# Kernel tuning notes

Hardware: AMD Instinct MI355X
Metric: run time of the kernel (lower is better)

## Reference

```python
import math
import jax, jax.numpy as jnp
import numpy as np

B, T, C, H = 2, 2048, 1024, 16
D = C // H


def _slopes(n):
    def p2(m):
        start = 2 ** (-(2 ** -(math.log2(m) - 3)))
        return [start * start ** i for i in range(m)]
    if math.log2(n).is_integer():
        return p2(n)
    c = 2 ** math.floor(math.log2(n))
    return p2(c) + _slopes(2 * c)[0::2][: n - c]


def setup_inputs() -> dict:
    key = jax.random.key(0)
    ks = jax.random.split(key, 9)
    std = 0.02
    x = jax.random.normal(ks[0], (B, T, C), dtype=jnp.float32)
    Wq = std * jax.random.normal(ks[1], (C, C), dtype=jnp.float32)
    Wk = std * jax.random.normal(ks[2], (C, C), dtype=jnp.float32)
    Wv = std * jax.random.normal(ks[3], (C, C), dtype=jnp.float32)
    # fc_resid init: std 0.02/sqrt(num_layers)
    Wo = (std / math.sqrt(24.0)) * jax.random.normal(ks[4], (C, C), dtype=jnp.float32)
    bq = jnp.zeros((C,), jnp.float32)
    bk = jnp.zeros((C,), jnp.float32)
    bv = jnp.zeros((C,), jnp.float32)
    bo = jnp.zeros((C,), jnp.float32)
    return {"x": x, "Wq": Wq, "bq": bq, "Wk": Wk, "bk": bk,
            "Wv": Wv, "bv": bv, "Wo": Wo, "bo": bo}


def reference(x, Wq, bq, Wk, bk, Wv, bv, Wo, bo):
    # projections -> [B, T, H, D]
    q = (x @ Wq + bq).reshape(B, T, H, D)
    k = (x @ Wk + bk).reshape(B, T, H, D)
    v = (x @ Wv + bv).reshape(B, T, H, D)

    scale = 1.0 / math.sqrt(D)
    att = jnp.einsum("bqhd,bkhd->bhqk", q, k) * scale  # [B,H,T,T]

    slopes = jnp.asarray(_slopes(H), dtype=jnp.float32)  # [H]
    i = jnp.arange(T)
    rel = i[None, :] - i[None, :].T  # rel[i,j] = j - i
    causal = rel <= 0  # j <= i
    # alibi bias: -tril(i - j) = tril(j - i), scaled per head
    alibi = slopes[:, None, None] * jnp.where(causal, rel, 0).astype(jnp.float32)

    att = att + alibi[None]  # broadcast over batch
    att = jnp.where(causal[None, None], att, -jnp.inf)
    att = jax.nn.softmax(att, axis=-1)

    y = jnp.einsum("bhqk,bkhd->bqhd", att, v).reshape(B, T, C)
    return y @ Wo + bo  # dropout p=0 (eval) is identity
```

## Files before the change

kernel.cpp:

```cpp
#include <hip/hip_runtime.h>
#include <hip/hip_bf16.h>

typedef __bf16 bf16;
typedef __bf16 bf16x4 __attribute__((ext_vector_type(4)));
typedef __bf16 bf16x8 __attribute__((ext_vector_type(8)));
typedef float floatx4 __attribute__((ext_vector_type(4)));
typedef short short4_ __attribute__((ext_vector_type(4)));

#define B_ 2
#define T_ 2048
#define C_ 1024
#define H_ 16
#define D_ 64
#define M_ 4096
#define QK_LD 2048

__device__ __forceinline__ void load_lds16(const void* g, void* l) {
  __builtin_amdgcn_global_load_lds(
      (const __attribute__((address_space(1))) unsigned int*)g,
      (__attribute__((address_space(3))) unsigned int*)l, 16, 0, 0);
}

__device__ __forceinline__ floatx4 mfma16(bf16x4 a, bf16x4 b, floatx4 c) {
#if __has_builtin(__builtin_amdgcn_mfma_f32_16x16x16_bf16)
  return __builtin_amdgcn_mfma_f32_16x16x16_bf16(a, b, c, 0, 0, 0);
#else
  return __builtin_amdgcn_mfma_f32_16x16x16bf16_1k(
      __builtin_bit_cast(short4_, a), __builtin_bit_cast(short4_, b), c, 0, 0, 0);
#endif
}

struct PrepArgs { const float* w[4]; bf16* wt[4]; const float* x; bf16* xb; };

__global__ __launch_bounds__(256)
void prep(PrepArgs p) {
  const int bid = blockIdx.x;
  if (bid < 4096) {
    __shared__ float tile[32][33];
    const int z = bid >> 10, xy = bid & 1023;
    const int bx = xy & 31, by = xy >> 5;
    const float* in = p.w[z];
    bf16* out = p.wt[z];
    int tx = threadIdx.x & 31, ty = threadIdx.x >> 5;
    int n0 = bx * 32, k0 = by * 32;
#pragma unroll
    for (int j = 0; j < 32; j += 8)
      tile[ty + j][tx] = in[(size_t)(k0 + ty + j) * C_ + n0 + tx];
    __syncthreads();
#pragma unroll
    for (int j = 0; j < 32; j += 8)
      out[(size_t)(n0 + ty + j) * C_ + k0 + tx] = (bf16)tile[tx][ty + j];
  } else {
    int i = ((bid - 4096) * 256 + threadIdx.x) * 8;
    float4 a = *(const float4*)(p.x + i);
    float4 b = *(const float4*)(p.x + i + 4);
    bf16x8 o;
    o[0] = (bf16)a.x; o[1] = (bf16)a.y; o[2] = (bf16)a.z; o[3] = (bf16)a.w;
    o[4] = (bf16)b.x; o[5] = (bf16)b.y; o[6] = (bf16)b.z; o[7] = (bf16)b.w;
    *(bf16x8*)(p.xb + i) = o;
  }
}

struct GQ {
  const bf16* A; const bf16* Bt;
  const float* bias[3];
  bf16* Cout; bf16* vt; int N; int K;
};

__global__ __launch_bounds__(256, 2)
void gemm128(GQ g) {
  __shared__ __align__(16) bf16 As[128 * 64];
  __shared__ __align__(16) bf16 Bs[128 * 64];
  const int tid = threadIdx.x;
  const int wave = tid >> 6, lane = tid & 63;
  const int quad = lane >> 4, l16 = lane & 15;
  const int m0 = blockIdx.y * 128, n0 = blockIdx.x * 128;
  const int wm = (wave >> 1) * 64, wn = (wave & 1) * 64;

  floatx4 acc[4][4] = {};

  int rA[4], cA[4];
#pragma unroll
  for (int t = 0; t < 4; ++t) {
    int pch = (wave * 4 + t) * 64 + lane;
    rA[t] = pch >> 3;
    cA[t] = (pch & 7) ^ (rA[t] & 7);
  }

  for (int k0 = 0; k0 < g.K; k0 += 64) {
    __syncthreads();
#pragma unroll
    for (int t = 0; t < 4; ++t) {
      load_lds16(g.A + (size_t)(m0 + rA[t]) * g.K + k0 + cA[t] * 8,
                 As + (wave * 4 + t) * 512);
      load_lds16(g.Bt + (size_t)(n0 + rA[t]) * g.K + k0 + cA[t] * 8,
                 Bs + (wave * 4 + t) * 512);
    }
    __builtin_amdgcn_s_waitcnt(0x0f70);
    __syncthreads();
#pragma unroll
    for (int s = 0; s < 2; ++s) {
      bf16x8 af[4], bfr[4];
#pragma unroll
      for (int i = 0; i < 4; ++i) {
        int mr = wm + i * 16 + l16;
        af[i] = *(const bf16x8*)(As + ((mr * 8) + ((s * 4 + quad) ^ (mr & 7))) * 8);
        int nr = wn + i * 16 + l16;
        bfr[i] = *(const bf16x8*)(Bs + ((nr * 8) + ((s * 4 + quad) ^ (nr & 7))) * 8);
      }
#pragma unroll
      for (int i = 0; i < 4; ++i)
#pragma unroll
        for (int j = 0; j < 4; ++j)
          acc[i][j] = __builtin_amdgcn_mfma_f32_16x16x32_bf16(af[i], bfr[j],
                                                              acc[i][j], 0, 0, 0);
    }
  }

  const bool vsplit = (n0 >= 2048);
#pragma unroll
  for (int j = 0; j < 4; ++j) {
    int col = n0 + wn + j * 16 + l16;
    const float* bp = g.bias[col >> 10];
    float bv = bp[col & 1023];
    if (vsplit) {
      int cv = col - 2048;
      bf16* dst0 = g.vt + ((size_t)((m0 >> 11) * 16 + (cv >> 6)) * 64 + (cv & 63)) * (size_t)T_
                   + (m0 & 2047) + wm + quad * 4;
#pragma unroll
      for (int i = 0; i < 4; ++i) {
        bf16x4 pk;
#pragma unroll
        for (int r = 0; r < 4; ++r) pk[r] = (bf16)(acc[i][j][r] + bv);
        *(bf16x4*)(dst0 + i * 16) = pk;
      }
    } else {
#pragma unroll
      for (int i = 0; i < 4; ++i) {
#pragma unroll
        for (int r = 0; r < 4; ++r) {
          int row = m0 + wm + i * 16 + quad * 4 + r;
          g.Cout[(size_t)row * g.N + col] = (bf16)(acc[i][j][r] + bv);
        }
      }
    }
  }
}

__global__ __launch_bounds__(256, 2)
void gemm_out(const bf16* __restrict__ A, const bf16* __restrict__ Bt,
              const float* __restrict__ bias, float* __restrict__ C) {
  __shared__ __align__(16) bf16 As[64 * 64];
  __shared__ __align__(16) bf16 Bs[128 * 64];
  const int tid = threadIdx.x;
  const int wave = tid >> 6, lane = tid & 63;
  const int quad = lane >> 4, l16 = lane & 15;
  const int m0 = blockIdx.y * 64, n0 = blockIdx.x * 128;
  const int wm = (wave >> 1) * 32, wn = (wave & 1) * 64;

  floatx4 acc[2][4] = {};

  int rA[2], cA[2], rB[4], cB[4];
#pragma unroll
  for (int t = 0; t < 2; ++t) {
    int p = t * 256 + tid;
    rA[t] = p >> 3; cA[t] = (p & 7) ^ (rA[t] & 7);
  }
#pragma unroll
  for (int t = 0; t < 4; ++t) {
    int p = t * 256 + tid;
    rB[t] = p >> 3; cB[t] = (p & 7) ^ (rB[t] & 7);
  }

  for (int k0 = 0; k0 < 1024; k0 += 64) {
    __syncthreads();
#pragma unroll
    for (int t = 0; t < 2; ++t)
      load_lds16(A + (size_t)(m0 + rA[t]) * 1024 + k0 + cA[t] * 8,
                 As + t * 2048 + wave * 512);
#pragma unroll
    for (int t = 0; t < 4; ++t)
      load_lds16(Bt + (size_t)(n0 + rB[t]) * 1024 + k0 + cB[t] * 8,
                 Bs + t * 2048 + wave * 512);
    __builtin_amdgcn_s_waitcnt(0x0f70);
    __syncthreads();
#pragma unroll
    for (int s = 0; s < 2; ++s) {
      bf16x8 af[2], bfr[4];
#pragma unroll
      for (int i = 0; i < 2; ++i) {
        int mr = wm + i * 16 + l16;
        af[i] = *(const bf16x8*)(As + ((mr * 8) + ((s * 4 + quad) ^ (mr & 7))) * 8);
      }
#pragma unroll
      for (int j = 0; j < 4; ++j) {
        int nr = wn + j * 16 + l16;
        bfr[j] = *(const bf16x8*)(Bs + ((nr * 8) + ((s * 4 + quad) ^ (nr & 7))) * 8);
      }
#pragma unroll
      for (int i = 0; i < 2; ++i)
#pragma unroll
        for (int j = 0; j < 4; ++j)
          acc[i][j] = __builtin_amdgcn_mfma_f32_16x16x32_bf16(af[i], bfr[j],
                                                              acc[i][j], 0, 0, 0);
    }
  }

#pragma unroll
  for (int j = 0; j < 4; ++j) {
    int col = n0 + wn + j * 16 + l16;
    float bv = bias[col];
#pragma unroll
    for (int i = 0; i < 2; ++i)
#pragma unroll
      for (int r = 0; r < 4; ++r) {
        int row = m0 + wm + i * 16 + quad * 4 + r;
        C[(size_t)row * 1024 + col] = acc[i][j][r] + bv;
      }
  }
}

__constant__ int yy_map[24] = {7, 8, 16, 9, 17, 6, 10, 18, 11, 19, 5, 12,
                               20, 13, 21, 4, 14, 22, 15, 23, 3, 2, 1, 0};

__global__ __launch_bounds__(512, 2)
void attn8(const bf16* __restrict__ qk, const bf16* __restrict__ vt,
           bf16* __restrict__ y, bf16* __restrict__ po, float* __restrict__ pl) {
  __shared__ __align__(16) bf16 smem[17408];
  const int tid = threadIdx.x, wave = tid >> 6, lane = tid & 63;
  const int quad = lane >> 4, l16 = lane & 15;
  const int qs = wave >> 1, kh = wave & 1;
  const int bh = blockIdx.x, b = bh >> 4, h = bh & 15;
  const int yy = yy_map[blockIdx.y];
  int qb, kbeg, kcnt, seg;
  if (yy < 8)       { qb = yy;      kbeg = 0;      kcnt = 2 * qb + 2; seg = -1; }
  else if (yy < 16) { qb = 23 - yy; kbeg = 0;      kcnt = qb + 1;     seg = 0;  }
  else              { qb = 31 - yy; kbeg = qb + 1; kcnt = qb + 1;     seg = 1;  }

  const float L2E = 1.4426950408889634f;
  const float slope2 = exp2f(-0.5f * (float)(h + 1)) * L2E;
  const float scl2 = 0.125f * L2E;
  const float M0 = 14.0f;

  const int rS = tid >> 3;
  const int cS = (tid & 7) ^ (rS & 7);
  const bf16* kbase = qk + (size_t)b * T_ * QK_LD + 1024 + h * 64;
  const bf16* vbase = vt + (size_t)bh * 64 * T_;

  const int q0 = qb * 128;
  const int w0 = q0 + qs * 32;

  bf16x8 qf[2][2];
#pragma unroll
  for (int qt = 0; qt < 2; ++qt)
#pragma unroll
    for (int s = 0; s < 2; ++s)
      qf[qt][s] = *(const bf16x8*)(qk +
          (size_t)(b * T_ + w0 + qt * 16 + l16) * QK_LD + h * 64 + s * 32 + quad * 8);

  const int qi0 = w0 + l16;
  float qoff[2];
  qoff[0] = slope2 * (float)qi0 + M0;
  qoff[1] = qoff[0] + slope2 * 16.0f;
  float kc[2][4];
#pragma unroll
  for (int kt = 0; kt < 2; ++kt)
#pragma unroll
    for (int r = 0; r < 4; ++r)
      kc[kt][r] = slope2 * (float)(kt * 16 + quad * 4 + r);

  floatx4 o[2][4];
#pragma unroll
  for (int qt = 0; qt < 2; ++qt)
#pragma unroll
    for (int n = 0; n < 4; ++n) o[qt][n] = (floatx4)0.f;
  float lsum[2] = {0.f, 0.f};

  load_lds16(kbase + (size_t)(kbeg * 64 + rS) * QK_LD + cS * 8, smem + wave * 512);
  load_lds16(vbase + (size_t)rS * T_ + kbeg * 64 + cS * 8, smem + 8192 + wave * 512);
  __builtin_amdgcn_s_waitcnt(0x0f70);
  __syncthreads();

  for (int it = 0; it < kcnt; ++it) {
    const int kj0 = (kbeg + it) * 64;
    const int cur = it & 1;

    if (it + 1 < kcnt) {
      const int nk = kj0 + 64;
      load_lds16(kbase + (size_t)(nk + rS) * QK_LD + cS * 8,
                 smem + (cur ^ 1) * 4096 + wave * 512);
      load_lds16(vbase + (size_t)rS * T_ + nk + cS * 8,
                 smem + 8192 + (cur ^ 1) * 4096 + wave * 512);
    }

    const bf16* Klc = smem + cur * 4096;
    const bf16* Vlc = smem + 8192 + cur * 4096;

    bf16x8 kf[2][2];
#pragma unroll
    for (int ss = 0; ss < 2; ++ss)
#pragma unroll
      for (int kt = 0; kt < 2; ++kt) {
        const int krow = kh * 32 + kt * 16 + l16;
        kf[ss][kt] = *(const bf16x8*)(Klc + krow * 64 +
                                      (((ss * 4 + quad) ^ (krow & 7)) * 8));
      }
    bf16x4 vfr[4][2];
#pragma unroll
    for (int nt = 0; nt < 4; ++nt) {
      const int drow = nt * 16 + l16;
#pragma unroll
      for (int kt = 0; kt < 2; ++kt) {
        const int chunk = (kh * 4 + kt * 2 + (quad >> 1)) ^ (drow & 7);
        vfr[nt][kt] = *(const bf16x4*)(Vlc + drow * 64 + chunk * 8 + (quad & 1) * 4);
      }
    }

    const int kbi = kj0 + kh * 32;
    const float kb = slope2 * (float)kbi;

#pragma unroll
    for (int qt = 0; qt < 2; ++qt) {
      const int rb = w0 + qt * 16;
      floatx4 st[2] = {};
#pragma unroll
      for (int ss = 0; ss < 2; ++ss)
#pragma unroll
        for (int kt = 0; kt < 2; ++kt)
          st[kt] = __builtin_amdgcn_mfma_f32_16x16x32_bf16(kf[ss][kt], qf[qt][ss],
                                                           st[kt], 0, 0, 0);

      const float bb = kb - qoff[qt];
      const int qi = qi0 + qt * 16;
      bf16x4 pb[2];
      if (kbi + 31 > rb) {
#pragma unroll
        for (int kt = 0; kt < 2; ++kt) {
#pragma unroll
          for (int r = 0; r < 4; ++r) {
            float p = __builtin_amdgcn_exp2f(
                fmaf(st[kt][r], scl2, bb + kc[kt][r]));
            if (kbi + kt * 16 + quad * 4 + r > qi) p = 0.f;
            lsum[qt] += p;
            pb[kt][r] = (bf16)p;
          }
        }
      } else {
#pragma unroll
        for (int kt = 0; kt < 2; ++kt) {
#pragma unroll
          for (int r = 0; r < 4; ++r) {
            float p = __builtin_amdgcn_exp2f(
                fmaf(st[kt][r], scl2, bb + kc[kt][r]));
            lsum[qt] += p;
            pb[kt][r] = (bf16)p;
          }
        }
      }

#pragma unroll
      for (int nt = 0; nt < 4; ++nt)
#pragma unroll
        for (int kt = 0; kt < 2; ++kt)
          o[qt][nt] = mfma16(vfr[nt][kt], pb[kt], o[qt][nt]);
    }

    __builtin_amdgcn_s_waitcnt(0x0f70);
    __syncthreads();
  }

  float* Cb = (float*)smem;
  if (kh == 1) {
#pragma unroll
    for (int qt = 0; qt < 2; ++qt) {
#pragma unroll
      for (int n = 0; n < 4; ++n)
        *(floatx4*)(Cb + (((qs * 2 + qt) * 4 + n) * 64 + lane) * 4) = o[qt][n];
      Cb[8192 + (qs * 2 + qt) * 64 + lane] = lsum[qt];
    }
  }
  __syncthreads();
  if (kh == 1) return;
#pragma unroll
  for (int qt = 0; qt < 2; ++qt) {
#pragma unroll
    for (int n = 0; n < 4; ++n)
      o[qt][n] += *(const floatx4*)(Cb + (((qs * 2 + qt) * 4 + n) * 64 + lane) * 4);
    lsum[qt] += Cb[8192 + (qs * 2 + qt) * 64 + lane];
    lsum[qt] += __shfl_xor(lsum[qt], 16);
    lsum[qt] += __shfl_xor(lsum[qt], 32);
  }

  if (seg < 0) {
#pragma unroll
    for (int qt = 0; qt < 2; ++qt) {
      const float inv = 1.f / lsum[qt];
      bf16* yp = y + (size_t)(b * T_ + w0 + qt * 16 + l16) * C_ + h * 64 + quad * 4;
#pragma unroll
      for (int nt = 0; nt < 4; ++nt) {
        bf16x4 pk;
#pragma unroll
        for (int r = 0; r < 4; ++r) pk[r] = (bf16)(o[qt][nt][r] * inv);
        *(bf16x4*)(yp + nt * 16) = pk;
      }
    }
  } else {
    const int pid = (bh * 8 + (qb - 8)) * 2 + seg;
    bf16* pob = po + (size_t)pid * 8192;
#pragma unroll
    for (int qt = 0; qt < 2; ++qt) {
#pragma unroll
      for (int half = 0; half < 2; ++half) {
        bf16x8 pk;
#pragma unroll
        for (int jj = 0; jj < 8; ++jj)
          pk[jj] = (bf16)o[qt][half * 2 + (jj >> 2)][jj & 3];
        *(bf16x8*)(pob + (qt * 2 + half) * 2048 + (qs * 64 + lane) * 8) = pk;
      }
      if (quad == 0)
        pl[pid * 128 + qs * 32 + qt * 16 + l16] = lsum[qt];
    }
  }
}

__global__ __launch_bounds__(256)
void combine(const bf16* __restrict__ po, const float* __restrict__ pl,
             bf16* __restrict__ y) {
  const int x = blockIdx.x;
  const int bh = x >> 3, qb = (x & 7) + 8;
  const int b = bh >> 4, h = bh & 15;
  const int pid0 = (bh * 8 + (qb - 8)) * 2;
  const bf16* p0 = po + (size_t)pid0 * 8192;
  const bf16* p1 = p0 + 8192;
  const int t = threadIdx.x;
  const int qs = t >> 6, quad = (t >> 4) & 3, l16 = t & 15;

  float linv[2];
  int row[2];
#pragma unroll
  for (int qt = 0; qt < 2; ++qt) {
    row[qt] = qs * 32 + qt * 16 + l16;
    linv[qt] = 1.f / (pl[pid0 * 128 + row[qt]] + pl[(pid0 + 1) * 128 + row[qt]]);
  }

#pragma unroll
  for (int qt = 0; qt < 2; ++qt)
#pragma unroll
    for (int half = 0; half < 2; ++half) {
      bf16x8 a = *(const bf16x8*)(p0 + (qt * 2 + half) * 2048 + t * 8);
      bf16x8 c = *(const bf16x8*)(p1 + (qt * 2 + half) * 2048 + t * 8);
#pragma unroll
      for (int g = 0; g < 2; ++g) {
        bf16x4 outv;
#pragma unroll
        for (int r = 0; r < 4; ++r)
          outv[r] = (bf16)(((float)a[g * 4 + r] + (float)c[g * 4 + r]) * linv[qt]);
        const int col = (half * 2 + g) * 16 + quad * 4;
        *(bf16x4*)(y + (size_t)(b * T_ + qb * 128 + row[qt]) * C_ + h * 64 + col) = outv;
      }
    }
}

extern "C" void kernel_launch(void* const* d_in, const int* in_sizes, int n_in,
                              void* d_out, int out_size, void* d_ws, size_t ws_size,
                              hipStream_t stream) {
  const float* x  = (const float*)d_in[0];
  const float* Wq = (const float*)d_in[1];
  const float* bq = (const float*)d_in[2];
  const float* Wk = (const float*)d_in[3];
  const float* bk = (const float*)d_in[4];
  const float* Wv = (const float*)d_in[5];
  const float* bv = (const float*)d_in[6];
  const float* Wo = (const float*)d_in[7];
  const float* bo = (const float*)d_in[8];

  bf16* ws  = (bf16*)d_ws;
  bf16* WtQ = ws;
  bf16* WtK = WtQ + (size_t)C_ * C_;
  bf16* WtV = WtK + (size_t)C_ * C_;
  bf16* WtO = WtV + (size_t)C_ * C_;
  bf16* xb  = WtO + (size_t)C_ * C_;
  bf16* qkb = xb + (size_t)M_ * C_;
  bf16* vtb = qkb + (size_t)M_ * 2 * C_;
  bf16* yb  = vtb + (size_t)M_ * C_;
  bf16* pob = yb + (size_t)M_ * C_;
  float* plb = (float*)(pob + (size_t)512 * 8192);

  PrepArgs pp;
  pp.w[0] = Wq; pp.w[1] = Wk; pp.w[2] = Wv; pp.w[3] = Wo;
  pp.wt[0] = WtQ; pp.wt[1] = WtK; pp.wt[2] = WtV; pp.wt[3] = WtO;
  pp.x = x; pp.xb = xb;
  prep<<<dim3(4096 + M_ * C_ / (256 * 8)), 256, 0, stream>>>(pp);

  GQ gq;
  gq.A = xb; gq.Bt = WtQ;
  gq.bias[0] = bq; gq.bias[1] = bk; gq.bias[2] = bv;
  gq.Cout = qkb; gq.vt = vtb; gq.N = 2 * C_; gq.K = C_;
  gemm128<<<dim3(24, 32), 256, 0, stream>>>(gq);

  attn8<<<dim3(32, 24), 512, 0, stream>>>(qkb, vtb, yb, pob, plb);
  combine<<<dim3(32 * 8), 256, 0, stream>>>(pob, plb, yb);

  gemm_out<<<dim3(8, 64), 256, 0, stream>>>(yb, WtO, bo, (float*)d_out);
}
```

Baseline: 179.6 us.

## Double-buffer two KV tiles per stage and permute V layout for 128-bit fragment loads

The attention loop now stages two 64-key K/V tiles per iteration, which halves the number of barrier/waitcnt points, and enlarges LDS to hold them. The QKV GEMM epilogue writes V^T with a permuted key order so each lane reads one 16-byte V fragment instead of two 8-byte ones, and the two halves feed the two MFMAs. It also raises wave priority around the MFMA/exp section. The cost is higher LDS use (64KB per block), which may cut occupancy, and handling of an odd tile count.

Measured after the change: 182.7 us. Within noise of the previous version (+1.7%).

```diff
diff --git a/kernel.cpp b/kernel.cpp
--- a/kernel.cpp
+++ b/kernel.cpp
@@ -28,6 +28,13 @@
   return __builtin_amdgcn_mfma_f32_16x16x16bf16_1k(
       __builtin_bit_cast(short4_, a), __builtin_bit_cast(short4_, b), c, 0, 0, 0);
 #endif
+}
+
+__device__ __forceinline__ bf16x4 lo4(bf16x8 v) {
+  return __builtin_shufflevector(v, v, 0, 1, 2, 3);
+}
+__device__ __forceinline__ bf16x4 hi4(bf16x8 v) {
+  return __builtin_shufflevector(v, v, 4, 5, 6, 7);
 }
 
 struct PrepArgs { const float* w[4]; bf16* wt[4]; const float* x; bf16* xb; };
@@ -125,14 +132,14 @@
     float bv = bp[col & 1023];
     if (vsplit) {
       int cv = col - 2048;
-      bf16* dst0 = g.vt + ((size_t)((m0 >> 11) * 16 + (cv >> 6)) * 64 + (cv & 63)) * (size_t)T_
-                   + (m0 & 2047) + wm + quad * 4;
+      bf16* dstb = g.vt + ((size_t)((m0 >> 11) * 16 + (cv >> 6)) * 64 + (cv & 63)) * (size_t)T_
+                   + (m0 & 2047) + wm + quad * 8;
 #pragma unroll
       for (int i = 0; i < 4; ++i) {
         bf16x4 pk;
 #pragma unroll
         for (int r = 0; r < 4; ++r) pk[r] = (bf16)(acc[i][j][r] + bv);
-        *(bf16x4*)(dst0 + i * 16) = pk;
+        *(bf16x4*)(dstb + (i >> 1) * 32 + (i & 1) * 4) = pk;
       }
     } else {
 #pragma unroll
@@ -226,7 +233,7 @@
 __global__ __launch_bounds__(512, 2)
 void attn8(const bf16* __restrict__ qk, const bf16* __restrict__ vt,
            bf16* __restrict__ y, bf16* __restrict__ po, float* __restrict__ pl) {
-  __shared__ __align__(16) bf16 smem[17408];
+  __shared__ __align__(16) bf16 smem[32768];
   const int tid = threadIdx.x, wave = tid >> 6, lane = tid & 63;
   const int quad = lane >> 4, l16 = lane & 15;
   const int qs = wave >> 1, kh = wave & 1;
@@ -276,93 +283,107 @@
     for (int n = 0; n < 4; ++n) o[qt][n] = (floatx4)0.f;
   float lsum[2] = {0.f, 0.f};
 
-  load_lds16(kbase + (size_t)(kbeg * 64 + rS) * QK_LD + cS * 8, smem + wave * 512);
-  load_lds16(vbase + (size_t)rS * T_ + kbeg * 64 + cS * 8, smem + 8192 + wave * 512);
+#pragma unroll
+  for (int s2 = 0; s2 < 2; ++s2) {
+    load_lds16(kbase + (size_t)((kbeg + s2) * 64 + rS) * QK_LD + cS * 8,
+               smem + s2 * 4096 + wave * 512);
+    load_lds16(vbase + (size_t)rS * T_ + (kbeg + s2) * 64 + cS * 8,
+               smem + 16384 + s2 * 4096 + wave * 512);
+  }
   __builtin_amdgcn_s_waitcnt(0x0f70);
   __syncthreads();
 
-  for (int it = 0; it < kcnt; ++it) {
-    const int kj0 = (kbeg + it) * 64;
+  const int nit = (kcnt + 1) >> 1;
+  for (int it = 0; it < nit; ++it) {
     const int cur = it & 1;
 
-    if (it + 1 < kcnt) {
-      const int nk = kj0 + 64;
-      load_lds16(kbase + (size_t)(nk + rS) * QK_LD + cS * 8,
-                 smem + (cur ^ 1) * 4096 + wave * 512);
-      load_lds16(vbase + (size_t)rS * T_ + nk + cS * 8,
-                 smem + 8192 + (cur ^ 1) * 4096 + wave * 512);
-    }
-
-    const bf16* Klc = smem + cur * 4096;
-    const bf16* Vlc = smem + 8192 + cur * 4096;
-
-    bf16x8 kf[2][2];
-#pragma unroll
-    for (int ss = 0; ss < 2; ++ss)
-#pragma unroll
-      for (int kt = 0; kt < 2; ++kt) {
-        const int krow = kh * 32 + kt * 16 + l16;
-        kf[ss][kt] = *(const bf16x8*)(Klc + krow * 64 +
-                                      (((ss * 4 + quad) ^ (krow & 7)) * 8));
-      }
-    bf16x4 vfr[4][2];
-#pragma unroll
-    for (int nt = 0; nt < 4; ++nt) {
-      const int drow = nt * 16 + l16;
-#pragma unroll
-      for (int kt = 0; kt < 2; ++kt) {
-        const int chunk = (kh * 4 + kt * 2 + (quad >> 1)) ^ (drow & 7);
-        vfr[nt][kt] = *(const bf16x4*)(Vlc + drow * 64 + chunk * 8 + (quad & 1) * 4);
-      }
-    }
-
-    const int kbi = kj0 + kh * 32;
-    const float kb = slope2 * (float)kbi;
-
-#pragma unroll
-    for (int qt = 0; qt < 2; ++qt) {
-      const int rb = w0 + qt * 16;
-      floatx4 st[2] = {};
-#pragma unroll
-      for (int ss = 0; ss < 2; ++ss)
-#pragma unroll
-        for (int kt = 0; kt < 2; ++kt)
-          st[kt] = __builtin_amdgcn_mfma_f32_16x16x32_bf16(kf[ss][kt], qf[qt][ss],
-                                                           st[kt], 0, 0, 0);
-
-      const float bb = kb - qoff[qt];
-      const int qi = qi0 + qt * 16;
-      bf16x4 pb[2];
-      if (kbi + 31 > rb) {
-#pragma unroll
-        for (int kt = 0; kt < 2; ++kt) {
-#pragma unroll
-          for (int r = 0; r < 4; ++r) {
-            float p = __builtin_amdgcn_exp2f(
-                fmaf(st[kt][r], scl2, bb + kc[kt][r]));
-            if (kbi + kt * 16 + quad * 4 + r > qi) p = 0.f;
-            lsum[qt] += p;
-            pb[kt][r] = (bf16)p;
+    if (it + 1 < nit) {
+      const int nt0 = kbeg + 2 * it + 2;
+#pragma unroll
+      for (int s2 = 0; s2 < 2; ++s2) {
+        load_lds16(kbase + (size_t)((nt0 + s2) * 64 + rS) * QK_LD + cS * 8,
+                   smem + (cur ^ 1) * 8192 + s2 * 4096 + wave * 512);
+        load_lds16(vbase + (size_t)rS * T_ + (nt0 + s2) * 64 + cS * 8,
+                   smem + 16384 + (cur ^ 1) * 8192 + s2 * 4096 + wave * 512);
+      }
+    }
+
+#pragma unroll
+    for (int sub = 0; sub < 2; ++sub) {
+      const int tile = 2 * it + sub;
+      if (tile < kcnt) {
+        const int kj0 = (kbeg + tile) * 64;
+        const bf16* Klc = smem + cur * 8192 + sub * 4096;
+        const bf16* Vlc = smem + 16384 + cur * 8192 + sub * 4096;
+
+        bf16x8 kf[2][2];
+#pragma unroll
+        for (int ss = 0; ss < 2; ++ss)
+#pragma unroll
+          for (int kt = 0; kt < 2; ++kt) {
+            const int krow = kh * 32 + kt * 16 + l16;
+            kf[ss][kt] = *(const bf16x8*)(Klc + krow * 64 +
+                                          (((ss * 4 + quad) ^ (krow & 7)) * 8));
+          }
+        bf16x8 vf8[4];
+#pragma unroll
+        for (int nt = 0; nt < 4; ++nt) {
+          const int drow = nt * 16 + l16;
+          vf8[nt] = *(const bf16x8*)(Vlc + drow * 64 +
+                                     (((kh * 4 + quad) ^ (drow & 7)) * 8));
+        }
+
+        const int kbi = kj0 + kh * 32;
+        const float kb = slope2 * (float)kbi;
+
+        __builtin_amdgcn_s_setprio(1);
+#pragma unroll
+        for (int qt = 0; qt < 2; ++qt) {
+          const int rb = w0 + qt * 16;
+          floatx4 st[2] = {};
+#pragma unroll
+          for (int ss = 0; ss < 2; ++ss)
+#pragma unroll
+            for (int kt = 0; kt < 2; ++kt)
+              st[kt] = __builtin_amdgcn_mfma_f32_16x16x32_bf16(kf[ss][kt], qf[qt][ss],
+                                                               st[kt], 0, 0, 0);
+
+          const float bb = kb - qoff[qt];
+          const int qi = qi0 + qt * 16;
+          bf16x4 pb[2];
+          if (kbi + 31 > rb) {
+#pragma unroll
+            for (int kt = 0; kt < 2; ++kt) {
+#pragma unroll
+              for (int r = 0; r < 4; ++r) {
+                float p = __builtin_amdgcn_exp2f(
+                    fmaf(st[kt][r], scl2, bb + kc[kt][r]));
+                if (kbi + kt * 16 + quad * 4 + r > qi) p = 0.f;
+                lsum[qt] += p;
+                pb[kt][r] = (bf16)p;
+              }
+            }
+          } else {
+#pragma unroll
+            for (int kt = 0; kt < 2; ++kt) {
+#pragma unroll
+              for (int r = 0; r < 4; ++r) {
+                float p = __builtin_amdgcn_exp2f(
+                    fmaf(st[kt][r], scl2, bb + kc[kt][r]));
+                lsum[qt] += p;
+                pb[kt][r] = (bf16)p;
+              }
+            }
+          }
+
+#pragma unroll
+          for (int nt = 0; nt < 4; ++nt) {
+            o[qt][nt] = mfma16(lo4(vf8[nt]), pb[0], o[qt][nt]);
+            o[qt][nt] = mfma16(hi4(vf8[nt]), pb[1], o[qt][nt]);
           }
         }
-      } else {
-#pragma unroll
-        for (int kt = 0; kt < 2; ++kt) {
-#pragma unroll
-          for (int r = 0; r < 4; ++r) {
-            float p = __builtin_amdgcn_exp2f(
-                fmaf(st[kt][r], scl2, bb + kc[kt][r]));
-            lsum[qt] += p;
-            pb[kt][r] = (bf16)p;
-          }
-        }
-      }
-
-#pragma unroll
-      for (int nt = 0; nt < 4; ++nt)
-#pragma unroll
-        for (int kt = 0; kt < 2; ++kt)
-          o[qt][nt] = mfma16(vfr[nt][kt], pb[kt], o[qt][nt]);
+        __builtin_amdgcn_s_setprio(0);
+      }
     }
 
     __builtin_amdgcn_s_waitcnt(0x0f70);
```
